# Kernel tuning notes

Measured on AMD Instinct MI355X. Metric: run time of the kernel, lower is better.

The kernel has to match this reference:

```python
import jax, jax.numpy as jnp
import numpy as np

N_NODES = 20000   # graph nodes (rows of x)
N_EDGES = 40000
NUM_ENT = 300000  # node_count: embedding table rows
EMB_DIM = 64
D = 2 * EMB_DIM           # self.emb_dim = 128
SE = int(0.36 * D)        # s_emb_dim = 46
TE = D - SE               # t_emb_dim = 82
F = 256                   # raw feature cols of x
HID = 128                 # n_hidden
OUT = 2


def setup_inputs() -> dict:
    key = jax.random.key(0)
    ks = jax.random.split(key, 24)
    def nrm(k, shape, fan_in):
        return jax.random.normal(k, shape, jnp.float32) / np.sqrt(fan_in)
    inp = {
        'x': jax.random.normal(ks[0], (N_NODES, F), jnp.float32),
        'heads': jax.random.randint(ks[1], (N_EDGES,), 0, NUM_ENT),
        'rels': jax.random.randint(ks[2], (N_EDGES,), 0, 4),
        'tails': jax.random.randint(ks[3], (N_EDGES,), 0, NUM_ENT),
        'weeks': jax.random.uniform(ks[4], (N_EDGES,), jnp.float32),
        'edge_src': jnp.sort(jax.random.randint(ks[5], (N_EDGES,), 0, N_NODES)),
        'edge_dst': jax.random.randint(ks[6], (N_EDGES,), 0, N_NODES),
        'node_type': jax.random.randint(ks[7], (N_NODES,), 0, 5),
        'edge_type': jax.random.randint(ks[8], (N_EDGES,), 0, 4),
        'edge_index': jax.random.randint(ks[9], (2, N_EDGES), 0, N_NODES),
        # learned parameters
        'ent_embs': nrm(ks[10], (NUM_ENT, SE), SE),
        'rel_embs': nrm(ks[11], (4, D), D),
        'w_freq': nrm(ks[12], (NUM_ENT, TE), TE),
        'w_phi': nrm(ks[13], (NUM_ENT, TE), TE),
        'w_amp': nrm(ks[14], (NUM_ENT, TE), TE),
        'Wih': nrm(ks[15], (4 * D, D), D),
        'Whh': nrm(ks[16], (4 * D, D), D),
        'bih': jnp.zeros((4 * D,), jnp.float32),
        'bhh': jnp.zeros((4 * D,), jnp.float32),
        'fc1_w': nrm(ks[17], (HID, F + D), F + D),
        'fc1_b': jnp.zeros((HID,), jnp.float32),
        'ln_g': jnp.ones((HID,), jnp.float32),
        'ln_b': jnp.zeros((HID,), jnp.float32),
        'out_w': nrm(ks[18], (OUT, HID), HID),
        'out_b': jnp.zeros((OUT,), jnp.float32),
    }
    return inp


def _lstm_last_per_segment(pre, seg, Whh, bhh):
    """Run one LSTM over edges sorted by seg, resetting state at group
    boundaries; return per-step hidden states and the scatter index that
    selects the last step of each group (others map to dummy row N_NODES).
    pre: [E, 4D] precomputed x @ Wih^T + bih (sorted by seg)."""
    reset = jnp.concatenate([jnp.ones((1,), bool), seg[1:] != seg[:-1]])
    def step(carry, inp):
        h, c = carry
        p, r = inp
        h = jnp.where(r, 0.0, h)
        c = jnp.where(r, 0.0, c)
        gates = p + h @ Whh.T + bhh
        i, f, g, o = jnp.split(gates, 4, axis=-1)
        c = jax.nn.sigmoid(f) * c + jax.nn.sigmoid(i) * jnp.tanh(g)
        h = jax.nn.sigmoid(o) * jnp.tanh(c)
        return (h, c), h
    zero = jnp.zeros((D,), pre.dtype)
    _, hs = jax.lax.scan(step, (zero, zero), (pre, reset))
    is_last = jnp.concatenate([seg[1:] != seg[:-1], jnp.ones((1,), bool)])
    idx = jnp.where(is_last, seg, N_NODES)  # dummy row for non-last steps
    return hs, idx


def reference(x, heads, rels, tails, weeks, edge_src, edge_dst, node_type,
              edge_type, edge_index, ent_embs, rel_embs, w_freq, w_phi, w_amp,
              Wih, Whh, bih, bhh, fc1_w, fc1_b, ln_g, ln_b, out_w, out_b):
    week = weeks.reshape(-1, 1)  # [E,1]
    # getEmbeddings: static entity emb + diachronic (amp*sin(freq*t+phi)) part
    h_t = w_amp[heads] * jnp.sin(w_freq[heads] * week + w_phi[heads])
    t_t = w_amp[tails] * jnp.sin(w_freq[tails] * week + w_phi[tails])
    h = jnp.concatenate([ent_embs[heads], h_t], axis=1)  # [E, D]
    t = jnp.concatenate([ent_embs[tails], t_t], axis=1)  # [E, D]
    r = rel_embs[rels]                                    # [E, D]
    scores = h * r * t                                    # [E, D]

    # Ragged per-group LSTM (src groups, then dst groups overwrite), fused
    # as a single segment-reset scan per pass. Input projection hoisted.
    pre = scores @ Wih.T + bih  # [E, 4D]
    emb = jnp.zeros((N_NODES + 1, D), scores.dtype)
    perm_s = jnp.argsort(edge_src)  # stable
    hs, idx = _lstm_last_per_segment(pre[perm_s], edge_src[perm_s], Whh, bhh)
    emb = emb.at[idx].set(hs)
    perm_d = jnp.argsort(edge_dst)
    hs, idx = _lstm_last_per_segment(pre[perm_d], edge_dst[perm_d], Whh, bhh)
    emb = emb.at[idx].set(hs)
    emb = emb[:N_NODES]

    # (hgtconv2 omitted: GeneralConv source unavailable; treated as identity)
    xc = jnp.concatenate([x, emb], axis=1)  # mask = arange(N): all rows
    h1 = xc @ fc1_w.T + fc1_b
    mu = jnp.mean(h1, axis=-1, keepdims=True)
    var = jnp.mean((h1 - mu) ** 2, axis=-1, keepdims=True)
    h1 = (h1 - mu) / jnp.sqrt(var + 1e-5) * ln_g + ln_b
    h1 = jax.nn.relu(h1)  # dropout: eval mode, identity
    return h1 @ out_w.T + out_b
```

## Files before the change

kernel.cpp:

```cpp
#include <hip/hip_runtime.h>
#include <math.h>

#define N_NODES 20000
#define N_EDGES 40000
#define SE 46
#define TE 82
#define NBLK 79

typedef short  s16x8 __attribute__((ext_vector_type(8)));
typedef short  s16x4 __attribute__((ext_vector_type(4)));
typedef float  f32x4 __attribute__((ext_vector_type(4)));

__device__ __forceinline__ float sigf(float x){ return 1.0f/(1.0f+__expf(-x)); }
__device__ __forceinline__ float tanh_f(float x){ return 1.0f - 2.0f/(__expf(2.0f*x)+1.0f); }
__device__ __forceinline__ int perm_out(int i){ return (i&3)*128 + (i>>2); }
__device__ __forceinline__ unsigned short f2bf(float f){
  unsigned u = __builtin_bit_cast(unsigned, f);
  unsigned r = (u + 0x7fff + ((u>>16)&1)) >> 16;
  return (unsigned short)r;
}
__device__ __forceinline__ float bf2f(short s){
  unsigned u = ((unsigned)(unsigned short)s) << 16;
  return __builtin_bit_cast(float, u);
}

__global__ void k_prepw(const float* __restrict__ in, short* __restrict__ out, int n){
  int i = blockIdx.x*blockDim.x + threadIdx.x;
  if (i < n) out[i] = (short)f2bf(in[i]);
}

__global__ void k_prepwih(const float* __restrict__ in, short* __restrict__ out){
  int idx = blockIdx.x*blockDim.x + threadIdx.x;
  if (idx < 512*128){
    int i = idx >> 7, k = idx & 127;
    out[idx] = (short)f2bf(in[perm_out(i)*128 + k]);
  }
}

__global__ __launch_bounds__(256) void k_gather(
    const int* __restrict__ heads, const int* __restrict__ rels,
    const int* __restrict__ tails, const float* __restrict__ weeks,
    const float* __restrict__ ent, const float* __restrict__ rel_embs,
    const float* __restrict__ wfreq, const float* __restrict__ wphi,
    const float* __restrict__ wamp, short* __restrict__ scores){
  int c = blockIdx.x*256 + threadIdx.x;
  int e = c >> 4, d0 = (c & 15) << 3;
  int hd = heads[e], tl = tails[e], rl = rels[e];
  float wk = weeks[e];
  float hv[8], tv[8];
  if (d0 + 8 <= SE){
    const float* hp = ent + (size_t)hd*SE + d0;
    const float* tp = ent + (size_t)tl*SE + d0;
    #pragma unroll
    for (int j=0;j<4;j++){
      float2 a = *(const float2*)(hp + j*2); hv[2*j]=a.x; hv[2*j+1]=a.y;
      float2 b = *(const float2*)(tp + j*2); tv[2*j]=b.x; tv[2*j+1]=b.y;
    }
  } else if (d0 >= 48){
    int dt = d0 - SE;
    const float *hf = wfreq + (size_t)hd*TE + dt, *hp2 = wphi + (size_t)hd*TE + dt, *ha = wamp + (size_t)hd*TE + dt;
    const float *tf = wfreq + (size_t)tl*TE + dt, *tp2 = wphi + (size_t)tl*TE + dt, *ta = wamp + (size_t)tl*TE + dt;
    #pragma unroll
    for (int j=0;j<4;j++){
      float2 f_h = *(const float2*)(hf + j*2);
      float2 p_h = *(const float2*)(hp2 + j*2);
      float2 a_h = *(const float2*)(ha + j*2);
      float2 f_t = *(const float2*)(tf + j*2);
      float2 p_t = *(const float2*)(tp2 + j*2);
      float2 a_t = *(const float2*)(ta + j*2);
      hv[2*j]   = a_h.x*__sinf(f_h.x*wk + p_h.x);
      hv[2*j+1] = a_h.y*__sinf(f_h.y*wk + p_h.y);
      tv[2*j]   = a_t.x*__sinf(f_t.x*wk + p_t.x);
      tv[2*j+1] = a_t.y*__sinf(f_t.y*wk + p_t.y);
    }
  } else {
    #pragma unroll
    for (int j=0;j<8;j++){
      int d = 40 + j;
      if (d < SE){
        hv[j] = ent[(size_t)hd*SE + d];
        tv[j] = ent[(size_t)tl*SE + d];
      } else {
        int dt = d - SE;
        hv[j] = wamp[(size_t)hd*TE+dt]*__sinf(wfreq[(size_t)hd*TE+dt]*wk + wphi[(size_t)hd*TE+dt]);
        tv[j] = wamp[(size_t)tl*TE+dt]*__sinf(wfreq[(size_t)tl*TE+dt]*wk + wphi[(size_t)tl*TE+dt]);
      }
    }
  }
  const float* rp = rel_embs + rl*128 + d0;
  float4 r0 = *(const float4*)rp, r1 = *(const float4*)(rp+4);
  float rv[8] = {r0.x,r0.y,r0.z,r0.w, r1.x,r1.y,r1.z,r1.w};
  s16x8 o;
  #pragma unroll
  for (int j=0;j<8;j++) o[j] = (short)f2bf(hv[j]*rv[j]*tv[j]);
  *(s16x8*)(scores + (size_t)e*128 + d0) = o;
}

__global__ __launch_bounds__(256) void k_pregemm(
    const short* __restrict__ scores, const short* __restrict__ WihB,
    const float* __restrict__ bih, const float* __restrict__ bhh,
    short* __restrict__ pre2b){
  __shared__ char As[32*256];
  int e0 = blockIdx.x * 32;
  int tid = threadIdx.x;
  #pragma unroll
  for (int q=0;q<2;q++){
    int c = tid + 256*q;
    int el = c >> 4, k8 = c & 15;
    s16x8 v = *(const s16x8*)(scores + (size_t)(e0+el)*128 + k8*8);
    *(s16x8*)(As + ((el*256 + k8*16) ^ ((el&7)<<4))) = v;
  }
  __syncthreads();
  int lane = tid & 63, w = tid >> 6;
  int cl = lane & 15, kq = lane >> 4;
  s16x8 a[2][4];
  #pragma unroll
  for (int ks=0;ks<4;ks++){
    int kb = ks*64 + kq*16;
    a[0][ks] = *(const s16x8*)(As + (((cl   )*256 + kb) ^ ((cl&7)<<4)));
    a[1][ks] = *(const s16x8*)(As + (((cl+16)*256 + kb) ^ (((cl+16)&7)<<4)));
  }
  f32x4 D[2][8];
  #pragma unroll
  for (int m=0;m<2;m++)
    #pragma unroll
    for (int i=0;i<8;i++) D[m][i] = (f32x4){0.f,0.f,0.f,0.f};
  #pragma unroll
  for (int i=0;i<8;i++){
    int n = w*128 + i*16 + cl;
    const short* bp = WihB + (size_t)n*128 + kq*8;
    #pragma unroll
    for (int ks=0;ks<4;ks++){
      s16x8 b = *(const s16x8*)(bp + ks*32);
      D[0][i] = __builtin_amdgcn_mfma_f32_16x16x32_bf16(a[0][ks], b, D[0][i], 0, 0, 0);
      D[1][i] = __builtin_amdgcn_mfma_f32_16x16x32_bf16(a[1][ks], b, D[1][i], 0, 0, 0);
    }
  }
  #pragma unroll
  for (int i=0;i<8;i++){
    int n = w*128 + i*16 + cl;
    int pn = perm_out(n);
    float bb = bih[pn] + bhh[pn];
    #pragma unroll
    for (int m=0;m<2;m++){
      #pragma unroll
      for (int q2=0;q2<4;q2++){
        int row = m*16 + kq*4 + q2;
        pre2b[(size_t)(e0+row)*512 + n] = (short)f2bf(D[m][i][q2] + bb);
      }
    }
  }
}

__global__ void k_hist(const int* __restrict__ src, const int* __restrict__ dst,
                       int* __restrict__ scnt, int* __restrict__ dcnt){
  int e = blockIdx.x*blockDim.x + threadIdx.x;
  if (e < N_EDGES){ atomicAdd(&scnt[src[e]],1); atomicAdd(&dcnt[dst[e]],1); }
}

__global__ void k_scan(const int* __restrict__ scnt, const int* __restrict__ dcnt,
                       int* __restrict__ sstart, int* __restrict__ dstart){
  const int* cnt = blockIdx.x ? dcnt : scnt;
  int* start = blockIdx.x ? dstart : sstart;
  const int CH = 20;
  int tid = threadIdx.x;
  int base = tid*CH;
  int v[CH]; int tsum = 0;
  #pragma unroll
  for (int j=0;j<CH;j++){ int i = base+j; v[j] = (i<N_NODES)? cnt[i] : 0; tsum += v[j]; }
  int lane = tid & 63, wv = tid >> 6;
  int incl = tsum;
  #pragma unroll
  for (int m=1;m<64;m<<=1){ int u = __shfl_up(incl, m); if (lane >= m) incl += u; }
  __shared__ int wsum[16], woff[16];
  if (lane==63) wsum[wv] = incl;
  __syncthreads();
  if (tid < 16){ int s=0; for (int k=0;k<tid;k++) s += wsum[k]; woff[tid]=s; }
  __syncthreads();
  int run = woff[wv] + incl - tsum;
  #pragma unroll
  for (int j=0;j<CH;j++){ int i = base+j; if (i<N_NODES) start[i] = run; run += v[j]; }
  if (tid == 1023) start[N_NODES] = run;
}

__global__ void k_scatter(const int* __restrict__ src, const int* __restrict__ dst,
                          const int* __restrict__ sstart, const int* __restrict__ dstart,
                          int* __restrict__ sc2, int* __restrict__ dc2,
                          int* __restrict__ slist, int* __restrict__ dlist){
  int e = blockIdx.x*blockDim.x + threadIdx.x;
  if (e < N_EDGES){
    int s = src[e]; int p  = sstart[s] + atomicAdd(&sc2[s],1); slist[p]=e;
    int d = dst[e]; int p2 = dstart[d] + atomicAdd(&dc2[d],1); dlist[p2]=e;
  }
}

__global__ void k_sortlists(const int* __restrict__ sstart, const int* __restrict__ dstart,
                            int* __restrict__ slist, int* __restrict__ dlist){
  int n = blockIdx.x*blockDim.x + threadIdx.x;
  if (n < N_NODES){
    #pragma unroll
    for (int pass=0; pass<2; pass++){
      const int* st = pass ? dstart : sstart;
      int* ls = pass ? dlist : slist;
      int a = st[n], b = st[n+1];
      for (int i=a+1;i<b;i++){
        int v = ls[i]; int j=i-1;
        while (j>=a && ls[j]>v){ ls[j+1]=ls[j]; j--; }
        ls[j+1]=v;
      }
    }
  }
}

__global__ void k_cbin1(const int* __restrict__ sstart, const int* __restrict__ dstart,
                        int* __restrict__ bhist){
  __shared__ int h[128];
  int tid = threadIdx.x, blk = blockIdx.x;
  if (tid < 128) h[tid] = 0;
  __syncthreads();
  int n = blk*256 + tid;
  if (n < N_NODES){
    int c  = sstart[n+1]-sstart[n];
    int c2 = dstart[n+1]-dstart[n];
    if (c>0 && c2==0) atomicAdd(&h[min(c,63)], 1);
    if (c2>0) atomicAdd(&h[64+min(c2,63)], 1);
  }
  __syncthreads();
  if (tid < 128) bhist[tid*NBLK + blk] = h[tid];
}

__global__ void k_cbin2(const int* __restrict__ bhist, int* __restrict__ boff,
                        int* __restrict__ nchains){
  const int S = 2*63*NBLK;
  const int CH = 10;
  int tid = threadIdx.x;
  int v[CH]; int tsum = 0;
  int binidx[CH];
  #pragma unroll
  for (int j=0;j<CH;j++){
    int s = tid*CH + j;
    int val = 0, bi = -1;
    if (s < S){
      int p = s / (63*NBLK);
      int r = s - p*63*NBLK;
      int li = r / NBLK;
      int b  = r - li*NBLK;
      int l  = 63 - li;
      bi = (p*64 + l)*NBLK + b;
      val = bhist[bi];
    }
    binidx[j] = bi; v[j] = val; tsum += val;
  }
  int lane = tid & 63, wv = tid >> 6;
  int incl = tsum;
  #pragma unroll
  for (int m=1;m<64;m<<=1){ int u = __shfl_up(incl, m); if (lane >= m) incl += u; }
  __shared__ int wsum[16], woff[16];
  __shared__ int pend[2];
  if (lane==63) wsum[wv] = incl;
  __syncthreads();
  if (tid < 16){ int s=0; for (int k=0;k<tid;k++) s += wsum[k]; woff[tid]=s; }
  __syncthreads();
  int run = woff[wv] + incl - tsum;
  #pragma unroll
  for (int j=0;j<CH;j++){
    int s = tid*CH + j;
    if (s < S){
      boff[binidx[j]] = run;
      run += v[j];
      if (s == 63*NBLK - 1) pend[0] = run;
      if (s == S - 1)       pend[1] = run;
    }
  }
  __syncthreads();
  if (tid == 0){
    nchains[0] = pend[0];
    nchains[1] = pend[1] - pend[0];
  }
}

__global__ void k_cbin3(const int* __restrict__ sstart, const int* __restrict__ dstart,
                        const int* __restrict__ boff, const int* __restrict__ nchains,
                        int* __restrict__ cnode, int* __restrict__ cstart,
                        int* __restrict__ clen){
  __shared__ int h[128];
  int tid = threadIdx.x, blk = blockIdx.x;
  if (tid < 128) h[tid] = 0;
  __syncthreads();
  int n = blk*256 + tid;
  int bin0=-1, bin1=-1, r0=0, r1=0, a0=0, c0=0, a1=0, c1=0;
  if (n < N_NODES){
    a0 = sstart[n]; c0 = sstart[n+1]-a0;
    a1 = dstart[n]; c1 = dstart[n+1]-a1;
    if (c0>0 && c1==0){ bin0 = min(c0,63);    r0 = atomicAdd(&h[bin0], 1); }
    if (c1>0)         { bin1 = 64+min(c1,63); r1 = atomicAdd(&h[bin1], 1); }
  }
  __syncthreads();
  int nch0 = nchains[0];
  if (bin0 >= 0){
    int pos = boff[bin0*NBLK + blk] + r0;
    cnode[pos] = n; cstart[pos] = a0; clen[pos] = c0;
  }
  if (bin1 >= 0){
    int pos = boff[bin1*NBLK + blk] + r1 - nch0;
    cnode[N_NODES+pos] = n; cstart[N_NODES+pos] = a1; clen[N_NODES+pos] = c1;
  }
}

#define LDS_H4 131072
#define LDS_META4 147456
#define LDSZ4 148480

__global__ __launch_bounds__(512, 1) void k_lstm5(
    const short* __restrict__ pre2b, const float* __restrict__ Whh,
    const int* __restrict__ cnode, const int* __restrict__ cstart,
    const int* __restrict__ clen, const int* __restrict__ nchains,
    const int* __restrict__ slist, const int* __restrict__ dlist,
    int* __restrict__ ctr, float* __restrict__ emb){
  extern __shared__ char smem[];
  int tid = threadIdx.x;
  int lane = tid & 63, wv = tid >> 6;
  int cl = lane & 15, kq = lane >> 4;
  int d_own = wv*16 + cl;
  #pragma unroll 1
  for (int q=0;q<16;q++){
    int c = q*512 + tid;
    int n = c >> 4, k8 = c & 15;
    const float* src = Whh + (size_t)n*128 + k8*8;
    s16x8 v8;
    #pragma unroll
    for (int j=0;j<8;j++) v8[j] = (short)f2bf(src[j]);
    int byt = (n*256 + k8*16) ^ ((n&7)<<4);
    *(s16x8*)(smem + byt) = v8;
  }
  int nch0 = nchains[0], nch1 = nchains[1];
  int B0 = (nch0+31)>>5, B1 = (nch1+31)>>5;
  int* M = (int*)(smem + LDS_META4);
  __syncthreads();
  while (true){
    if (tid==0) M[160] = atomicAdd(ctr, 1);
    __syncthreads();
    int nb = M[160];
    if (nb >= B0 + B1) break;
    int pass = (nb >= B0) ? 1 : 0;
    int batch = pass ? nb - B0 : nb;
    int b0 = batch << 5;
    int nch = pass ? nch1 : nch0;
    const int* list = pass ? dlist : slist;
    if (tid < 32){
      int j = b0 + tid;
      int valid = (j < nch);
      int ci = pass*N_NODES + j;
      int st = valid ? cstart[ci] : 0;
      int ln = valid ? clen[ci] : 0;
      M[tid] = ln; M[32+tid] = st; M[128+tid] = valid ? cnode[ci] : -1;
      M[64+tid] = (ln > 0) ? list[st]   : 0;
      M[96+tid] = (ln > 1) ? list[st+1] : 0;
    }
    {
      unsigned long long* hz = (unsigned long long*)(smem + LDS_H4 + tid*16);
      hz[0] = 0ull; hz[1] = 0ull;
    }
    float cst[8]  = {0.f,0.f,0.f,0.f,0.f,0.f,0.f,0.f};
    float hreg[8] = {0.f,0.f,0.f,0.f,0.f,0.f,0.f,0.f};
    __syncthreads();
    int mylen[8];
    #pragma unroll
    for (int m=0;m<2;m++)
      #pragma unroll
      for (int q=0;q<4;q++) mylen[m*4+q] = M[m*16 + kq*4 + q];
    int ml = 0;
    #pragma unroll 1
    for (int j=0;j<32;j++) ml = max(ml, M[j]);
    s16x4 pvc[8];
    #pragma unroll
    for (int m=0;m<2;m++)
      #pragma unroll
      for (int q=0;q<4;q++){
        int r = m*16 + kq*4 + q;
        pvc[m*4+q] = *(const s16x4*)(pre2b + (size_t)M[64+r]*512 + d_own*4);
      }
    int cur = 0;
    for (int t=0; t<ml; t++){
      s16x4 pvn[8];
      const int* eidN = M + 64 + (((t+1)&1)<<5);
      #pragma unroll
      for (int m=0;m<2;m++)
        #pragma unroll
        for (int q=0;q<4;q++){
          int r = m*16 + kq*4 + q;
          pvn[m*4+q] = *(const s16x4*)(pre2b + (size_t)eidN[r]*512 + d_own*4);
        }
      f32x4 D[2][4];
      #pragma unroll
      for (int m=0;m<2;m++)
        #pragma unroll
        for (int i=0;i<4;i++) D[m][i] = (f32x4){0.f,0.f,0.f,0.f};
      char* Hc = smem + LDS_H4 + cur*8192;
      #pragma unroll
      for (int ks=0; ks<4; ks++){
        int kb = ks*64 + kq*16;
        s16x8 a0 = *(const s16x8*)(Hc + (((cl   )*256 + kb) ^ ((cl&7)<<4)));
        s16x8 a1 = *(const s16x8*)(Hc + (((cl+16)*256 + kb) ^ (((cl+16)&7)<<4)));
        #pragma unroll
        for (int i=0;i<4;i++){
          int n = i*128 + d_own;
          s16x8 b = *(const s16x8*)(smem + ((n*256 + kb) ^ ((n&7)<<4)));
          D[0][i] = __builtin_amdgcn_mfma_f32_16x16x32_bf16(a0, b, D[0][i], 0, 0, 0);
          D[1][i] = __builtin_amdgcn_mfma_f32_16x16x32_bf16(a1, b, D[1][i], 0, 0, 0);
        }
      }
      char* Hn = smem + LDS_H4 + (cur^1)*8192;
      #pragma unroll
      for (int m=0;m<2;m++)
        #pragma unroll
        for (int q=0;q<4;q++){
          int r = m*16 + kq*4 + q;
          if (t < mylen[m*4+q]){
            s16x4 p = pvc[m*4+q];
            float gi = D[m][0][q] + bf2f(p[0]);
            float gf = D[m][1][q] + bf2f(p[1]);
            float gg = D[m][2][q] + bf2f(p[2]);
            float go = D[m][3][q] + bf2f(p[3]);
            int idx = m*4+q;
            cst[idx] = sigf(gf)*cst[idx] + sigf(gi)*tanh_f(gg);
            float h = sigf(go)*tanh_f(cst[idx]);
            hreg[idx] = h;
            *(short*)(Hn + ((r*256 + d_own*2) ^ ((r&7)<<4))) = (short)f2bf(h);
          }
        }
      if (tid < 32){
        int ln = M[tid];
        M[64 + ((t&1)<<5) + tid] = (t+2 < ln) ? list[M[32+tid] + t+2] : 0;
      }
      __syncthreads();
      #pragma unroll
      for (int i=0;i<8;i++) pvc[i] = pvn[i];
      cur ^= 1;
    }
    #pragma unroll
    for (int m=0;m<2;m++)
      #pragma unroll
      for (int q=0;q<4;q++){
        int r = m*16 + kq*4 + q;
        int n = M[128+r];
        if (mylen[m*4+q] > 0 && n >= 0){
          emb[(size_t)n*128 + d_own] = hreg[m*4+q];
        }
      }
    __syncthreads();
  }
}

__global__ __launch_bounds__(512) void k_mlp2(
    const float* __restrict__ x, const float* __restrict__ emb,
    const short* __restrict__ fc1wbf, const float* __restrict__ fc1b,
    const float* __restrict__ lng, const float* __restrict__ lnb,
    const float* __restrict__ outw, const float* __restrict__ outb,
    float* __restrict__ out){
  __shared__ char As[32*768];
  __shared__ float hbuf[32][132];
  int tid = threadIdx.x;
  int lane = tid & 63, w = tid >> 6;
  int base = blockIdx.x * 32;
  #pragma unroll
  for (int q=0;q<3;q++){
    int i = tid + 512*q;
    int r = i / 48, c = i - r*48;
    const float* src = (c < 32) ? (x + (size_t)(base+r)*256 + c*8)
                                : (emb + (size_t)(base+r)*128 + (c-32)*8);
    float4 v0 = *(const float4*)src;
    float4 v1 = *(const float4*)(src+4);
    s16x8 v8;
    v8[0]=(short)f2bf(v0.x); v8[1]=(short)f2bf(v0.y); v8[2]=(short)f2bf(v0.z); v8[3]=(short)f2bf(v0.w);
    v8[4]=(short)f2bf(v1.x); v8[5]=(short)f2bf(v1.y); v8[6]=(short)f2bf(v1.z); v8[7]=(short)f2bf(v1.w);
    *(s16x8*)(As + ((r*768 + c*16) ^ ((r&7)<<4))) = v8;
  }
  __syncthreads();
  int cl = lane & 15, kq = lane >> 4;
  f32x4 D0 = {0.f,0.f,0.f,0.f}, D1 = {0.f,0.f,0.f,0.f};
  const short* bp = fc1wbf + (size_t)(w*16 + cl)*384 + kq*8;
  #pragma unroll
  for (int ks=0; ks<12; ks++){
    s16x8 b = *(const s16x8*)(bp + ks*32);
    int kb = ks*64 + kq*16;
    s16x8 a0 = *(const s16x8*)(As + (((cl   )*768 + kb) ^ ((cl&7)<<4)));
    s16x8 a1 = *(const s16x8*)(As + (((cl+16)*768 + kb) ^ (((cl+16)&7)<<4)));
    D0 = __builtin_amdgcn_mfma_f32_16x16x32_bf16(a0, b, D0, 0, 0, 0);
    D1 = __builtin_amdgcn_mfma_f32_16x16x32_bf16(a1, b, D1, 0, 0, 0);
  }
  int col = w*16 + cl;
  float bb = fc1b[col];
  #pragma unroll
  for (int q=0;q<4;q++){
    hbuf[kq*4+q][col]    = D0[q] + bb;
    hbuf[16+kq*4+q][col] = D1[q] + bb;
  }
  __syncthreads();
  int sub = lane >> 4, l16 = lane & 15;
  int nd = w*4 + sub;
  float v[8];
  float s = 0.f;
  #pragma unroll
  for (int j=0;j<8;j++){ v[j] = hbuf[nd][l16*8+j]; s += v[j]; }
  #pragma unroll
  for (int m=1;m<16;m<<=1) s += __shfl_xor(s, m);
  float mu = s * (1.f/128.f);
  float va = 0.f;
  #pragma unroll
  for (int j=0;j<8;j++){ float dm = v[j]-mu; va += dm*dm; }
  #pragma unroll
  for (int m=1;m<16;m<<=1) va += __shfl_xor(va, m);
  float rstd = rsqrtf(va*(1.f/128.f) + 1e-5f);
  float o0=0.f, o1=0.f;
  #pragma unroll
  for (int j=0;j<8;j++){
    int c = l16*8+j;
    float h1 = (v[j]-mu)*rstd*lng[c] + lnb[c];
    h1 = fmaxf(h1, 0.f);
    o0 += h1*outw[c]; o1 += h1*outw[128+c];
  }
  #pragma unroll
  for (int m=1;m<16;m<<=1){ o0 += __shfl_xor(o0,m); o1 += __shfl_xor(o1,m); }
  if (l16==0){
    out[(size_t)(base+nd)*2]   = o0 + outb[0];
    out[(size_t)(base+nd)*2+1] = o1 + outb[1];
  }
}

extern "C" void kernel_launch(void* const* d_in, const int* in_sizes, int n_in,
                              void* d_out, int out_size, void* d_ws, size_t ws_size,
                              hipStream_t stream){
  const float* x      = (const float*)d_in[0];
  const int*   heads  = (const int*)d_in[1];
  const int*   rels   = (const int*)d_in[2];
  const int*   tails  = (const int*)d_in[3];
  const float* weeks  = (const float*)d_in[4];
  const int*   esrc   = (const int*)d_in[5];
  const int*   edst   = (const int*)d_in[6];
  const float* ent    = (const float*)d_in[10];
  const float* rel_e  = (const float*)d_in[11];
  const float* wfreq  = (const float*)d_in[12];
  const float* wphi   = (const float*)d_in[13];
  const float* wamp   = (const float*)d_in[14];
  const float* Wih    = (const float*)d_in[15];
  const float* Whh    = (const float*)d_in[16];
  const float* bih    = (const float*)d_in[17];
  const float* bhh    = (const float*)d_in[18];
  const float* fc1w   = (const float*)d_in[19];
  const float* fc1b   = (const float*)d_in[20];
  const float* lng    = (const float*)d_in[21];
  const float* lnb    = (const float*)d_in[22];
  const float* outw   = (const float*)d_in[23];
  const float* outb   = (const float*)d_in[24];
  float* out = (float*)d_out;

  char* ws = (char*)d_ws;
  size_t off = 0;
  auto alloc = [&](size_t bytes){ void* p = ws + off; off += (bytes + 255) & ~(size_t)255; return p; };
  short* pre2b  = (short*)alloc((size_t)N_EDGES*512*2);
  short* scores = (short*)alloc((size_t)N_EDGES*128*2);
  short* WihB   = (short*)alloc(512*128*2);
  short* fc1wbf = (short*)alloc(128*384*2);
  float* emb    = (float*)alloc((size_t)N_NODES*128*4);
  int* sstart   = (int*)alloc((N_NODES+1)*4);
  int* dstart   = (int*)alloc((N_NODES+1)*4);
  int* zreg     = (int*)alloc((size_t)(4*N_NODES + 3)*4);
  int* scnt = zreg, *dcnt = zreg+N_NODES, *sc2 = zreg+2*N_NODES, *dc2 = zreg+3*N_NODES;
  int* nchains  = zreg + 4*N_NODES;
  int* ctr      = nchains + 2;
  int* bhist    = (int*)alloc((size_t)128*NBLK*4);
  int* boff     = (int*)alloc((size_t)128*NBLK*4);
  int* slist    = (int*)alloc(N_EDGES*4);
  int* dlist    = (int*)alloc(N_EDGES*4);
  int* cnode    = (int*)alloc((size_t)2*N_NODES*4);
  int* cstart   = (int*)alloc((size_t)2*N_NODES*4);
  int* clen     = (int*)alloc((size_t)2*N_NODES*4);

  hipMemsetAsync(zreg, 0, (size_t)(4*N_NODES + 3)*4, stream);
  hipMemsetAsync(emb, 0, (size_t)N_NODES*128*4, stream);

  hipFuncSetAttribute((const void*)k_lstm5, hipFuncAttributeMaxDynamicSharedMemorySize, LDSZ4);

  k_prepwih<<<(512*128+255)/256, 256, 0, stream>>>(Wih, WihB);
  k_prepw<<<(128*384+255)/256, 256, 0, stream>>>(fc1w, fc1wbf, 128*384);

  k_gather<<<N_EDGES*16/256, 256, 0, stream>>>(heads, rels, tails, weeks, ent, rel_e,
                                               wfreq, wphi, wamp, scores);
  k_pregemm<<<N_EDGES/32, 256, 0, stream>>>(scores, WihB, bih, bhh, pre2b);
  k_hist<<<(N_EDGES+255)/256, 256, 0, stream>>>(esrc, edst, scnt, dcnt);
  k_scan<<<2, 1024, 0, stream>>>(scnt, dcnt, sstart, dstart);
  k_scatter<<<(N_EDGES+255)/256, 256, 0, stream>>>(esrc, edst, sstart, dstart, sc2, dc2, slist, dlist);
  k_sortlists<<<(N_NODES+255)/256, 256, 0, stream>>>(sstart, dstart, slist, dlist);
  k_cbin1<<<NBLK, 256, 0, stream>>>(sstart, dstart, bhist);
  k_cbin2<<<1, 1024, 0, stream>>>(bhist, boff, nchains);
  k_cbin3<<<NBLK, 256, 0, stream>>>(sstart, dstart, boff, nchains, cnode, cstart, clen);
  k_lstm5<<<256, 512, LDSZ4, stream>>>(pre2b, Whh, cnode, cstart, clen, nchains,
                                       slist, dlist, ctr, emb);
  k_mlp2<<<N_NODES/32, 512, 0, stream>>>(x, emb, fc1wbf, fc1b, lng, lnb, outw, outb, out);
}
```

Before: 188.6 us.

## Hold recurrent LSTM weights in registers and merge weight-prep kernels

The recurrent Whh matrix is pre-converted to bf16 once in a merged prep kernel, and each LSTM thread now loads its B-operand fragments into registers at kernel start. This replaces the per-block bf16 conversion and the 128KB LDS staging. Each time step's MFMA then reads weights from registers instead of LDS, which removes LDS traffic on the serial recurrence. Shared memory drops to about 16KB plus metadata. The cost is 64 extra VGPRs per thread, which may raise register pressure under the 512-thread launch bound.

```diff
diff --git a/kernel.cpp b/kernel.cpp
--- a/kernel.cpp
+++ b/kernel.cpp
@@ -24,16 +24,20 @@
   return __builtin_bit_cast(float, u);
 }
 
-__global__ void k_prepw(const float* __restrict__ in, short* __restrict__ out, int n){
-  int i = blockIdx.x*blockDim.x + threadIdx.x;
-  if (i < n) out[i] = (short)f2bf(in[i]);
-}
-
-__global__ void k_prepwih(const float* __restrict__ in, short* __restrict__ out){
+__global__ void k_prep(const float* __restrict__ Wih, const float* __restrict__ Whh,
+                       const float* __restrict__ fc1w,
+                       short* __restrict__ WihB, short* __restrict__ WhhB2,
+                       short* __restrict__ fc1wbf){
   int idx = blockIdx.x*blockDim.x + threadIdx.x;
-  if (idx < 512*128){
+  if (idx < 65536){
     int i = idx >> 7, k = idx & 127;
-    out[idx] = (short)f2bf(in[perm_out(i)*128 + k]);
+    WihB[idx] = (short)f2bf(Wih[perm_out(i)*128 + k]);
+  } else if (idx < 131072){
+    int j = idx - 65536;
+    WhhB2[j] = (short)f2bf(Whh[j]);
+  } else if (idx < 180224){
+    int j = idx - 131072;
+    fc1wbf[j] = (short)f2bf(fc1w[j]);
   }
 }
 
@@ -307,36 +311,26 @@
   }
 }
 
-#define LDS_H4 131072
-#define LDS_META4 147456
-#define LDSZ4 148480
-
-__global__ __launch_bounds__(512, 1) void k_lstm5(
-    const short* __restrict__ pre2b, const float* __restrict__ Whh,
+__global__ __launch_bounds__(512, 1) void k_lstm6(
+    const short* __restrict__ pre2b, const short* __restrict__ WhhB2,
     const int* __restrict__ cnode, const int* __restrict__ cstart,
     const int* __restrict__ clen, const int* __restrict__ nchains,
     const int* __restrict__ slist, const int* __restrict__ dlist,
     int* __restrict__ ctr, float* __restrict__ emb){
-  extern __shared__ char smem[];
+  __shared__ char Hb[2][8192];
+  __shared__ int M[161];
   int tid = threadIdx.x;
   int lane = tid & 63, wv = tid >> 6;
   int cl = lane & 15, kq = lane >> 4;
   int d_own = wv*16 + cl;
-  #pragma unroll 1
-  for (int q=0;q<16;q++){
-    int c = q*512 + tid;
-    int n = c >> 4, k8 = c & 15;
-    const float* src = Whh + (size_t)n*128 + k8*8;
-    s16x8 v8;
-    #pragma unroll
-    for (int j=0;j<8;j++) v8[j] = (short)f2bf(src[j]);
-    int byt = (n*256 + k8*16) ^ ((n&7)<<4);
-    *(s16x8*)(smem + byt) = v8;
-  }
+  s16x8 wf[4][4];
+  #pragma unroll
+  for (int i=0;i<4;i++)
+    #pragma unroll
+    for (int ks=0;ks<4;ks++)
+      wf[i][ks] = *(const s16x8*)(WhhB2 + (size_t)(i*128 + d_own)*128 + ks*32 + kq*8);
   int nch0 = nchains[0], nch1 = nchains[1];
   int B0 = (nch0+31)>>5, B1 = (nch1+31)>>5;
-  int* M = (int*)(smem + LDS_META4);
-  __syncthreads();
   while (true){
     if (tid==0) M[160] = atomicAdd(ctr, 1);
     __syncthreads();
@@ -357,10 +351,8 @@
       M[64+tid] = (ln > 0) ? list[st]   : 0;
       M[96+tid] = (ln > 1) ? list[st+1] : 0;
     }
-    {
-      unsigned long long* hz = (unsigned long long*)(smem + LDS_H4 + tid*16);
-      hz[0] = 0ull; hz[1] = 0ull;
-    }
+    *(unsigned long long*)(&Hb[0][tid*16])   = 0ull;
+    *(unsigned long long*)(&Hb[0][tid*16+8]) = 0ull;
     float cst[8]  = {0.f,0.f,0.f,0.f,0.f,0.f,0.f,0.f};
     float hreg[8] = {0.f,0.f,0.f,0.f,0.f,0.f,0.f,0.f};
     __syncthreads();
@@ -396,7 +388,7 @@
       for (int m=0;m<2;m++)
         #pragma unroll
         for (int i=0;i<4;i++) D[m][i] = (f32x4){0.f,0.f,0.f,0.f};
-      char* Hc = smem + LDS_H4 + cur*8192;
+      char* Hc = Hb[cur];
       #pragma unroll
       for (int ks=0; ks<4; ks++){
         int kb = ks*64 + kq*16;
@@ -404,13 +396,11 @@
         s16x8 a1 = *(const s16x8*)(Hc + (((cl+16)*256 + kb) ^ (((cl+16)&7)<<4)));
         #pragma unroll
         for (int i=0;i<4;i++){
-          int n = i*128 + d_own;
-          s16x8 b = *(const s16x8*)(smem + ((n*256 + kb) ^ ((n&7)<<4)));
-          D[0][i] = __builtin_amdgcn_mfma_f32_16x16x32_bf16(a0, b, D[0][i], 0, 0, 0);
-          D[1][i] = __builtin_amdgcn_mfma_f32_16x16x32_bf16(a1, b, D[1][i], 0, 0, 0);
+          D[0][i] = __builtin_amdgcn_mfma_f32_16x16x32_bf16(a0, wf[i][ks], D[0][i], 0, 0, 0);
+          D[1][i] = __builtin_amdgcn_mfma_f32_16x16x32_bf16(a1, wf[i][ks], D[1][i], 0, 0, 0);
         }
       }
-      char* Hn = smem + LDS_H4 + (cur^1)*8192;
+      char* Hn = Hb[cur^1];
       #pragma unroll
       for (int m=0;m<2;m++)
         #pragma unroll
@@ -561,6 +551,7 @@
   short* pre2b  = (short*)alloc((size_t)N_EDGES*512*2);
   short* scores = (short*)alloc((size_t)N_EDGES*128*2);
   short* WihB   = (short*)alloc(512*128*2);
+  short* WhhB2  = (short*)alloc(512*128*2);
   short* fc1wbf = (short*)alloc(128*384*2);
   float* emb    = (float*)alloc((size_t)N_NODES*128*4);
   int* sstart   = (int*)alloc((N_NODES+1)*4);
@@ -580,10 +571,7 @@
   hipMemsetAsync(zreg, 0, (size_t)(4*N_NODES + 3)*4, stream);
   hipMemsetAsync(emb, 0, (size_t)N_NODES*128*4, stream);
 
-  hipFuncSetAttribute((const void*)k_lstm5, hipFuncAttributeMaxDynamicSharedMemorySize, LDSZ4);
-
-  k_prepwih<<<(512*128+255)/256, 256, 0, stream>>>(Wih, WihB);
-  k_prepw<<<(128*384+255)/256, 256, 0, stream>>>(fc1w, fc1wbf, 128*384);
+  k_prep<<<(180224+255)/256, 256, 0, stream>>>(Wih, Whh, fc1w, WihB, WhhB2, fc1wbf);
 
   k_gather<<<N_EDGES*16/256, 256, 0, stream>>>(heads, rels, tails, weeks, ent, rel_e,
                                                wfreq, wphi, wamp, scores);
@@ -595,7 +583,7 @@
   k_cbin1<<<NBLK, 256, 0, stream>>>(sstart, dstart, bhist);
   k_cbin2<<<1, 1024, 0, stream>>>(bhist, boff, nchains);
   k_cbin3<<<NBLK, 256, 0, stream>>>(sstart, dstart, boff, nchains, cnode, cstart, clen);
-  k_lstm5<<<256, 512, LDSZ4, stream>>>(pre2b, Whh, cnode, cstart, clen, nchains,
-                                       slist, dlist, ctr, emb);
+  k_lstm6<<<256, 512, 0, stream>>>(pre2b, WhhB2, cnode, cstart, clen, nchains,
+                                   slist, dlist, ctr, emb);
   k_mlp2<<<N_NODES/32, 512, 0, stream>>>(x, emb, fc1wbf, fc1b, lng, lnb, outw, outb, out);
 }
```

After: 181.1 us. 1.04x faster.
